# Kernel optimization log

Measured on AMD Instinct MI355X. Metric: run time of the kernel, lower is better.

Reference implementation:

```python
import jax, jax.numpy as jnp
import numpy as np

B, N, H = 2, 4096, 1024
HEADS, DHEAD, M = 16, 64, 256
KERNEL_EPS = 1e-3


def setup_inputs() -> dict:
    key = jax.random.key(0)
    ks = jax.random.split(key, 10)
    w = lambda k, shp: jax.random.normal(k, shp, dtype=jnp.float32) * 0.02
    return {
        "hidden_states": jax.random.normal(ks[0], (B, N, H), dtype=jnp.float32),
        "Wq": w(ks[1], (H, H)), "bq": jnp.zeros((H,), jnp.float32),
        "Wk": w(ks[2], (H, H)), "bk": jnp.zeros((H,), jnp.float32),
        "Wv": w(ks[3], (H, H)), "bv": jnp.zeros((H,), jnp.float32),
        "Wo": w(ks[4], (H, H)), "bo": jnp.zeros((H,), jnp.float32),
        "proj": jax.random.normal(ks[5], (M, DHEAD), dtype=jnp.float32),
    }


def _split_heads(x):
    b, n, _ = x.shape
    return x.reshape(b, n, HEADS, DHEAD).transpose(0, 2, 1, 3)  # [b,h,n,d]


def _softmax_kernel(data, proj, is_query):
    # data: [b,h,n,d]; proj: [m,d]
    data_normalizer = DHEAD ** (-0.25)
    data_dash = jnp.einsum('bhnd,md->bhnm', data_normalizer * data, proj)
    diag_data = -0.5 * jnp.sum(data * data, axis=-1, keepdims=True)  # [b,h,n,1]
    if is_query:
        # argmax over a size-1 last dim -> stabilizer == diag_data itself
        stab = diag_data
    else:
        stab = jnp.max(diag_data)
    kernel_out = jnp.exp(diag_data + (data_dash - stab))  # exp kernel: exp(h + x)
    return (M ** (-0.5)) * (kernel_out + KERNEL_EPS)


def _performer_forward(hidden_states, Wq, bq, Wk, bk, Wv, bv, Wo, bo, proj):
    q = _split_heads(jnp.einsum('bni,oi->bno', hidden_states, Wq) + bq)
    k = _split_heads(jnp.einsum('bni,oi->bno', hidden_states, Wk) + bk)
    v = _split_heads(jnp.einsum('bni,oi->bno', hidden_states, Wv) + bv)

    qf = _softmax_kernel(q, proj, is_query=True)   # [b,h,n,m]
    kf = _softmax_kernel(k, proj, is_query=False)  # [b,h,n,m]

    # linear_attention (non-causal FAVOR+)
    k_cumsum = kf.sum(axis=-2)                                   # [b,h,m]
    d_inv = 1.0 / jnp.einsum('bhnm,bhm->bhn', qf, k_cumsum)      # [b,h,n]
    context = jnp.einsum('bhnm,bhne->bhme', kf, v)               # [b,h,m,d]
    out = jnp.einsum('bhme,bhnm,bhn->bhne', context, qf, d_inv)  # [b,h,n,d]

    out = out.transpose(0, 2, 1, 3).reshape(hidden_states.shape[0], -1, H)
    return jnp.einsum('bni,oi->bno', out, Wo) + bo


def reference(hidden_states, Wq, bq, Wk, bk, Wv, bv, Wo, bo, proj):
    return _performer_forward(hidden_states, Wq, bq, Wk, bk, Wv, bv, Wo, bo, proj)
```

## Files before the change

kernel.cpp:

```cpp
#include <hip/hip_runtime.h>
#include <math.h>

#define B_      2
#define N_      4096
#define H_      1024
#define HEADS_  16
#define DH_     64
#define M_      256
#define NSPLIT  8
#define EPAD    80

constexpr float NORMALIZER = 0.35355339059327373f;
constexpr float RATIO      = 0.0625f;
constexpr float KEPS       = 1e-3f;

typedef __bf16 bf16x8 __attribute__((ext_vector_type(8)));
typedef __bf16 bf16x4 __attribute__((ext_vector_type(4)));
typedef float  f32x4  __attribute__((ext_vector_type(4)));

__global__ __launch_bounds__(256) void split_bf16(
    const float* __restrict__ src, __bf16* __restrict__ hi, __bf16* __restrict__ lo)
{
    int i = blockIdx.x * 256 + threadIdx.x;
    float4 v = ((const float4*)src)[i];
    float vv[4] = {v.x, v.y, v.z, v.w};
    bf16x4 h, l;
#pragma unroll
    for (int j = 0; j < 4; ++j) {
        __bf16 hh = (__bf16)vv[j];
        h[j] = hh;
        l[j] = (__bf16)(vv[j] - (float)hh);
    }
    ((bf16x4*)hi)[i] = h;
    ((bf16x4*)lo)[i] = l;
}

__global__ __launch_bounds__(256) void split_w(
    const float* __restrict__ W0, const float* __restrict__ W1,
    const float* __restrict__ W2, const float* __restrict__ W3,
    __bf16* __restrict__ hi, __bf16* __restrict__ lo)
{
    const float* src = W0;
    if (blockIdx.y == 1) src = W1;
    else if (blockIdx.y == 2) src = W2;
    else if (blockIdx.y == 3) src = W3;
    int i = blockIdx.x * 256 + threadIdx.x;
    size_t o = (size_t)blockIdx.y * 262144 + i;
    float4 v = ((const float4*)src)[i];
    float vv[4] = {v.x, v.y, v.z, v.w};
    bf16x4 h, l;
#pragma unroll
    for (int j = 0; j < 4; ++j) {
        __bf16 hh = (__bf16)vv[j];
        h[j] = hh;
        l[j] = (__bf16)(vv[j] - (float)hh);
    }
    ((bf16x4*)hi)[o] = h;
    ((bf16x4*)lo)[o] = l;
}

template<bool BF16OUT>
__global__ __launch_bounds__(512, 4) void gemm_mfma3(
    const __bf16* __restrict__ Ah, const __bf16* __restrict__ Al,
    const __bf16* __restrict__ Bh0, const __bf16* __restrict__ Bl0,
    const __bf16* __restrict__ Bh1, const __bf16* __restrict__ Bl1,
    const __bf16* __restrict__ Bh2, const __bf16* __restrict__ Bl2,
    const float* __restrict__ bi0, const float* __restrict__ bi1, const float* __restrict__ bi2,
    float* __restrict__ C0,
    __bf16* __restrict__ Ch0, __bf16* __restrict__ Cl0,
    __bf16* __restrict__ Ch1, __bf16* __restrict__ Cl1,
    __bf16* __restrict__ Ch2, __bf16* __restrict__ Cl2)
{
    const __bf16* Bh = Bh0; const __bf16* Bl = Bl0; const float* bias = bi0;
    __bf16* Ch = Ch0; __bf16* Cl = Cl0;
    if (blockIdx.z == 1) { Bh = Bh1; Bl = Bl1; bias = bi1; Ch = Ch1; Cl = Cl1; }
    else if (blockIdx.z == 2) { Bh = Bh2; Bl = Bl2; bias = bi2; Ch = Ch2; Cl = Cl2; }

    __shared__ alignas(16) __bf16 lds[2][4][128 * 32];

    const int t    = threadIdx.x;
    const int lane = t & 63;
    const int lm   = lane & 15;
    const int lq   = lane >> 4;
    const int w    = t >> 6;
    const int wm   = (w >> 2) * 64;
    const int wn   = (w & 3) * 32;

    const int wg = blockIdx.x + 8 * blockIdx.y;
    const int sw = (wg & 7) * 64 + (wg >> 3);
    const int n0 = (sw & 7) * 128;
    const int m0 = (sw >> 3) * 128;
    const int K    = 1024;
    const int NK   = 32;

    const int tw = w >> 1;
    const int hw = w & 1;
    const __bf16* mysrc = (tw == 0) ? Ah : (tw == 1) ? Al : (tw == 2) ? Bh : Bl;
    const int     rbase = ((tw < 2) ? m0 : n0) + hw * 64;
    const int rsub   = lane >> 2;
    const int slot   = lane & 3;
    const int schunk = slot ^ ((lane >> 3) & 3);
    const __bf16* gbase = mysrc + (size_t)(rbase + rsub) * K + schunk * 8;

    f32x4 acc[4][2];
#pragma unroll
    for (int i = 0; i < 4; ++i)
#pragma unroll
        for (int j = 0; j < 2; ++j) acc[i][j] = (f32x4){0.f, 0.f, 0.f, 0.f};

    const int swz = (lq ^ ((lm >> 1) & 3)) * 8;

    auto stage = [&](int buf, int k0) {
#pragma unroll
        for (int c = 0; c < 4; ++c) {
            const __bf16* g = gbase + (size_t)c * 16 * K + k0;
            __builtin_amdgcn_global_load_lds(
                (const __attribute__((address_space(1))) void*)g,
                (__attribute__((address_space(3))) void*)&lds[buf][tw][(hw * 64 + c * 16) * 32],
                16, 0, 0);
        }
    };

    auto compute = [&](int p) {
        const __bf16* tAh = lds[p][0];
        const __bf16* tAl = lds[p][1];
        const __bf16* tBh = lds[p][2];
        const __bf16* tBl = lds[p][3];
        bf16x8 bh[2], bl[2];
#pragma unroll
        for (int j = 0; j < 2; ++j) {
            int off = (wn + j * 16 + lm) * 32 + swz;
            bh[j] = *(const bf16x8*)&tBh[off];
            bl[j] = *(const bf16x8*)&tBl[off];
        }
#pragma unroll
        for (int i = 0; i < 4; ++i) {
            int off = (wm + i * 16 + lm) * 32 + swz;
            bf16x8 ah = *(const bf16x8*)&tAh[off];
            bf16x8 al = *(const bf16x8*)&tAl[off];
#pragma unroll
            for (int j = 0; j < 2; ++j) {
                acc[i][j] = __builtin_amdgcn_mfma_f32_16x16x32_bf16(ah, bh[j], acc[i][j], 0, 0, 0);
                acc[i][j] = __builtin_amdgcn_mfma_f32_16x16x32_bf16(al, bh[j], acc[i][j], 0, 0, 0);
                acc[i][j] = __builtin_amdgcn_mfma_f32_16x16x32_bf16(ah, bl[j], acc[i][j], 0, 0, 0);
            }
        }
    };

    stage(0, 0);
    int p = 0;
#pragma unroll 1
    for (int kk = 0; kk < NK - 1; ++kk) {
        stage(p ^ 1, (kk + 1) * 32);
        asm volatile("s_waitcnt vmcnt(4)" ::: "memory");
        asm volatile("s_barrier" ::: "memory");
        compute(p);
        asm volatile("s_barrier" ::: "memory");
        p ^= 1;
    }
    asm volatile("s_waitcnt vmcnt(0)" ::: "memory");
    asm volatile("s_barrier" ::: "memory");
    compute(p);

    float bsr[2];
#pragma unroll
    for (int j = 0; j < 2; ++j) bsr[j] = bias[n0 + wn + j * 16 + lm];
#pragma unroll
    for (int i = 0; i < 4; ++i)
#pragma unroll
        for (int r = 0; r < 4; ++r) {
            int rowm = m0 + wm + i * 16 + lq * 4 + r;
#pragma unroll
            for (int j = 0; j < 2; ++j) {
                int col = n0 + wn + j * 16 + lm;
                float o = acc[i][j][r] + bsr[j];
                if (BF16OUT) {
                    __bf16 hh = (__bf16)o;
                    Ch[(size_t)rowm * 1024 + col] = hh;
                    Cl[(size_t)rowm * 1024 + col] = (__bf16)(o - (float)hh);
                } else {
                    C0[(size_t)rowm * 1024 + col] = o;
                }
            }
        }
}

__global__ __launch_bounds__(256) void diag_kernel(
    const __bf16* __restrict__ Kh, const __bf16* __restrict__ Kl,
    float* __restrict__ diag, float* __restrict__ partials)
{
    int gt = blockIdx.x * 256 + threadIdx.x;
    int r  = gt >> 2;
    int q  = gt & 3;
    const bf16x8* ph = (const bf16x8*)(Kh + (size_t)r * 64 + q * 16);
    const bf16x8* pl = (const bf16x8*)(Kl + (size_t)r * 64 + q * 16);
    float s = 0.f;
#pragma unroll
    for (int i = 0; i < 2; ++i) {
        bf16x8 vh = ph[i], vl = pl[i];
#pragma unroll
        for (int j = 0; j < 8; ++j) {
            float x = (float)vh[j] + (float)vl[j];
            s += x * x;
        }
    }
    s += __shfl_xor(s, 1);
    s += __shfl_xor(s, 2);
    float d = -0.5f * s;
    if (q == 0) {
        int h = r & 15, bn = r >> 4;
        int n = bn & 4095, b = bn >> 12;
        diag[(((size_t)b * 16 + h) << 12) + n] = d;
    }
    __shared__ float red[256];
    red[threadIdx.x] = d;
    __syncthreads();
    for (int s2 = 128; s2 > 0; s2 >>= 1) {
        if (threadIdx.x < s2) red[threadIdx.x] = fmaxf(red[threadIdx.x], red[threadIdx.x + s2]);
        __syncthreads();
    }
    if (threadIdx.x == 0) partials[blockIdx.x] = red[0];
}

__global__ __launch_bounds__(256) void reduce_stab(
    const float* __restrict__ partials, float* __restrict__ stab, int n)
{
    float m = -3.0e38f;
    for (int i = threadIdx.x; i < n; i += 256) m = fmaxf(m, partials[i]);
    __shared__ float red[256];
    red[threadIdx.x] = m;
    __syncthreads();
    for (int s2 = 128; s2 > 0; s2 >>= 1) {
        if (threadIdx.x < s2) red[threadIdx.x] = fmaxf(red[threadIdx.x], red[threadIdx.x + s2]);
        __syncthreads();
    }
    if (threadIdx.x == 0) stab[0] = red[0];
}

__global__ __launch_bounds__(256) void ctx_mfma(
    const __bf16* __restrict__ Kh, const __bf16* __restrict__ Kl,
    const __bf16* __restrict__ Vh, const __bf16* __restrict__ Vl,
    const __bf16* __restrict__ projH, const __bf16* __restrict__ projL,
    const float* __restrict__ diag, const float* __restrict__ stabp,
    float* __restrict__ ctxp)
{
    __shared__ alignas(16) char ldsbuf[59904];
    __shared__ float dg[64];
    __bf16* kfTh = (__bf16*)ldsbuf;
    __bf16* kfTl = kfTh + 9216;
    __bf16* vTh  = kfTl + 9216;
    __bf16* vTl  = vTh + 5760;
    float*  ctxe = (float*)ldsbuf;

    const int t    = threadIdx.x;
    const int lane = t & 63;
    const int w    = t >> 6;
    const int lm   = lane & 15;
    const int lq   = lane >> 4;
    const int bh   = blockIdx.z;
    const int b    = bh >> 4, h = bh & 15;
    const int mh   = blockIdx.y;
    const int slice = blockIdx.x;
    const int mwave = mh * 128 + w * 32;
    const float stab = stabp[0];
    const size_t rowbase = (size_t)b * N_ * H_ + (size_t)h * DH_;
    const float* diag_bh = diag + (size_t)bh * N_;

    for (int idx = t; idx < 16 * 72; idx += 256) {
        int e = 64 + idx / 72, n = idx % 72;
        vTh[e * 72 + n] = (e == 64 && n < 64) ? (__bf16)1.0f : (__bf16)0.0f;
        vTl[e * 72 + n] = (__bf16)0.0f;
    }

    bf16x8 ph[2][2], pl[2][2];
#pragma unroll
    for (int mf = 0; mf < 2; ++mf)
#pragma unroll
        for (int ks = 0; ks < 2; ++ks) {
            size_t pa = (size_t)(mwave + mf * 16 + lm) * 64 + ks * 32 + lq * 8;
            ph[mf][ks] = *(const bf16x8*)(projH + pa);
            pl[mf][ks] = *(const bf16x8*)(projL + pa);
        }

    f32x4 acc[2][5];
#pragma unroll
    for (int mf = 0; mf < 2; ++mf)
#pragma unroll
        for (int ef = 0; ef < 5; ++ef) acc[mf][ef] = (f32x4){0.f, 0.f, 0.f, 0.f};

    for (int tile = 0; tile < 8; ++tile) {
        const int n0 = slice * (N_ / NSPLIT) + tile * 64;
        __syncthreads();

        {
            int nl = t >> 2, dc = (t & 3) * 16;
            size_t va = rowbase + (size_t)(n0 + nl) * H_ + dc;
            bf16x8 v0 = *(const bf16x8*)(Vh + va);
            bf16x8 v1 = *(const bf16x8*)(Vh + va + 8);
            bf16x8 u0 = *(const bf16x8*)(Vl + va);
            bf16x8 u1 = *(const bf16x8*)(Vl + va + 8);
#pragma unroll
            for (int j = 0; j < 8; ++j) {
                vTh[(dc + j) * 72 + nl]     = v0[j];
                vTh[(dc + 8 + j) * 72 + nl] = v1[j];
                vTl[(dc + j) * 72 + nl]     = u0[j];
                vTl[(dc + 8 + j) * 72 + nl] = u1[j];
            }
        }
        if (t < 64) dg[t] = diag_bh[n0 + t] - stab;

        f32x4 dsh[4][2];
#pragma unroll
        for (int nf = 0; nf < 4; ++nf) {
#pragma unroll
            for (int mf = 0; mf < 2; ++mf) dsh[nf][mf] = (f32x4){0.f, 0.f, 0.f, 0.f};
            bf16x8 ah[2], al[2];
#pragma unroll
            for (int ks = 0; ks < 2; ++ks) {
                size_t ka = rowbase + (size_t)(n0 + nf * 16 + lm) * H_ + ks * 32 + lq * 8;
                ah[ks] = *(const bf16x8*)(Kh + ka);
                al[ks] = *(const bf16x8*)(Kl + ka);
            }
#pragma unroll
            for (int mf = 0; mf < 2; ++mf)
#pragma unroll
                for (int ks = 0; ks < 2; ++ks) {
                    dsh[nf][mf] = __builtin_amdgcn_mfma_f32_16x16x32_bf16(ah[ks], ph[mf][ks], dsh[nf][mf], 0, 0, 0);
                    dsh[nf][mf] = __builtin_amdgcn_mfma_f32_16x16x32_bf16(al[ks], ph[mf][ks], dsh[nf][mf], 0, 0, 0);
                    dsh[nf][mf] = __builtin_amdgcn_mfma_f32_16x16x32_bf16(ah[ks], pl[mf][ks], dsh[nf][mf], 0, 0, 0);
                }
        }

        __syncthreads();

#pragma unroll
        for (int nf = 0; nf < 4; ++nf) {
            float4 dgv = *(const float4*)&dg[nf * 16 + lq * 4];
            float dga[4] = {dgv.x, dgv.y, dgv.z, dgv.w};
#pragma unroll
            for (int mf = 0; mf < 2; ++mf) {
                int mrow = w * 32 + mf * 16 + lm;
                bf16x4 vh_, vl_;
#pragma unroll
                for (int r = 0; r < 4; ++r) {
                    float kf = RATIO * (__expf(dga[r] + NORMALIZER * dsh[nf][mf][r]) + KEPS);
                    __bf16 hh = (__bf16)kf;
                    vh_[r] = hh;
                    vl_[r] = (__bf16)(kf - (float)hh);
                }
                int nbase = nf * 16 + lq * 4;
                *(bf16x4*)&kfTh[mrow * 72 + nbase] = vh_;
                *(bf16x4*)&kfTl[mrow * 72 + nbase] = vl_;
            }
        }

#pragma unroll
        for (int ks = 0; ks < 2; ++ks) {
#pragma unroll
            for (int mf = 0; mf < 2; ++mf) {
                bf16x8 af = *(const bf16x8*)&kfTh[(w * 32 + mf * 16 + lm) * 72 + ks * 32 + lq * 8];
                bf16x8 afl = *(const bf16x8*)&kfTl[(w * 32 + mf * 16 + lm) * 72 + ks * 32 + lq * 8];
#pragma unroll
                for (int ef = 0; ef < 5; ++ef) {
                    bf16x8 bfh = *(const bf16x8*)&vTh[(ef * 16 + lm) * 72 + ks * 32 + lq * 8];
                    bf16x8 bfl = *(const bf16x8*)&vTl[(ef * 16 + lm) * 72 + ks * 32 + lq * 8];
                    acc[mf][ef] = __builtin_amdgcn_mfma_f32_16x16x32_bf16(af,  bfh, acc[mf][ef], 0, 0, 0);
                    acc[mf][ef] = __builtin_amdgcn_mfma_f32_16x16x32_bf16(afl, bfh, acc[mf][ef], 0, 0, 0);
                    acc[mf][ef] = __builtin_amdgcn_mfma_f32_16x16x32_bf16(af,  bfl, acc[mf][ef], 0, 0, 0);
                }
            }
        }
    }

    __syncthreads();
#pragma unroll
    for (int mf = 0; mf < 2; ++mf)
#pragma unroll
        for (int ef = 0; ef < 5; ++ef)
#pragma unroll
            for (int r = 0; r < 4; ++r) {
                int ml = w * 32 + mf * 16 + lq * 4 + r;
                int e  = ef * 16 + lm;
                ctxe[ml * 81 + e] = acc[mf][ef][r];
            }
    __syncthreads();
    const size_t SLICE = (size_t)(B_ * HEADS_) * EPAD * M_;
    const size_t obase = (size_t)slice * SLICE + (size_t)bh * EPAD * M_;
    for (int i = t; i < EPAD * 128; i += 256) {
        int e = i >> 7, ml = i & 127;
        ctxp[obase + (size_t)e * M_ + mh * 128 + ml] = ctxe[ml * 81 + e];
    }
}

__global__ __launch_bounds__(256) void ctx_reduce(
    const float* __restrict__ ctxp, __bf16* __restrict__ ctxTh, __bf16* __restrict__ ctxTl)
{
    int idx = blockIdx.x * 256 + threadIdx.x;
    const size_t SLICE = (size_t)(B_ * HEADS_) * EPAD * M_;
    float s = 0.f;
#pragma unroll
    for (int k = 0; k < NSPLIT; ++k) s += ctxp[(size_t)k * SLICE + idx];
    __bf16 hh = (__bf16)s;
    ctxTh[idx] = hh;
    ctxTl[idx] = (__bf16)(s - (float)hh);
}

__global__ __launch_bounds__(256) void out_mfma(
    const __bf16* __restrict__ Qh, const __bf16* __restrict__ Ql,
    const __bf16* __restrict__ projH, const __bf16* __restrict__ projL,
    const __bf16* __restrict__ ctxTh, const __bf16* __restrict__ ctxTl,
    __bf16* __restrict__ attnH, __bf16* __restrict__ attnL)
{
    __shared__ alignas(16) __bf16 qfh[4][16][72];
    __shared__ alignas(16) __bf16 qfl[4][16][72];

    const int t    = threadIdx.x;
    const int lane = t & 63;
    const int w    = t >> 6;
    const int lm   = lane & 15;
    const int lq   = lane >> 4;
    const int bh   = blockIdx.y;
    const int b    = bh >> 4, h = bh & 15;
    const int nw   = blockIdx.x * 64 + w * 16;
    const size_t rowbase = (size_t)b * N_ * H_ + (size_t)h * DH_;

    bf16x8 qh_[2], ql_[2];
#pragma unroll
    for (int ks = 0; ks < 2; ++ks) {
        size_t qa = rowbase + (size_t)(nw + lm) * H_ + ks * 32 + lq * 8;
        qh_[ks] = *(const bf16x8*)(Qh + qa);
        ql_[ks] = *(const bf16x8*)(Ql + qa);
    }

    const __bf16* cth = ctxTh + (size_t)bh * EPAD * M_;
    const __bf16* ctl = ctxTl + (size_t)bh * EPAD * M_;

    f32x4 accO[5];
#pragma unroll
    for (int ef = 0; ef < 5; ++ef) accO[ef] = (f32x4){0.f, 0.f, 0.f, 0.f};

    for (int mc = 0; mc < 4; ++mc) {
        const int m0 = mc * 64;
        f32x4 dsh[4];
#pragma unroll
        for (int mf = 0; mf < 4; ++mf) {
            dsh[mf] = (f32x4){0.f, 0.f, 0.f, 0.f};
#pragma unroll
            for (int ks = 0; ks < 2; ++ks) {
                size_t pa = (size_t)(m0 + mf * 16 + lm) * 64 + ks * 32 + lq * 8;
                bf16x8 ph = *(const bf16x8*)(projH + pa);
                bf16x8 pl = *(const bf16x8*)(projL + pa);
                dsh[mf] = __builtin_amdgcn_mfma_f32_16x16x32_bf16(qh_[ks], ph, dsh[mf], 0, 0, 0);
                dsh[mf] = __builtin_amdgcn_mfma_f32_16x16x32_bf16(ql_[ks], ph, dsh[mf], 0, 0, 0);
                dsh[mf] = __builtin_amdgcn_mfma_f32_16x16x32_bf16(qh_[ks], pl, dsh[mf], 0, 0, 0);
            }
        }
#pragma unroll
        for (int mf = 0; mf < 4; ++mf)
#pragma unroll
            for (int r = 0; r < 4; ++r) {
                float qf = RATIO * (__expf(NORMALIZER * dsh[mf][r]) + KEPS);
                __bf16 hh = (__bf16)qf;
                int nloc = lq * 4 + r;
                qfh[w][nloc][mf * 16 + lm] = hh;
                qfl[w][nloc][mf * 16 + lm] = (__bf16)(qf - (float)hh);
            }
#pragma unroll
        for (int ks = 0; ks < 2; ++ks) {
            bf16x8 af  = *(const bf16x8*)&qfh[w][lm][ks * 32 + lq * 8];
            bf16x8 afl = *(const bf16x8*)&qfl[w][lm][ks * 32 + lq * 8];
#pragma unroll
            for (int ef = 0; ef < 5; ++ef) {
                size_t ca = (size_t)(ef * 16 + lm) * M_ + m0 + ks * 32 + lq * 8;
                bf16x8 bfh = *(const bf16x8*)(cth + ca);
                bf16x8 bfl = *(const bf16x8*)(ctl + ca);
                accO[ef] = __builtin_amdgcn_mfma_f32_16x16x32_bf16(af,  bfh, accO[ef], 0, 0, 0);
                accO[ef] = __builtin_amdgcn_mfma_f32_16x16x32_bf16(afl, bfh, accO[ef], 0, 0, 0);
                accO[ef] = __builtin_amdgcn_mfma_f32_16x16x32_bf16(af,  bfl, accO[ef], 0, 0, 0);
            }
        }
    }

    float dinv[4];
#pragma unroll
    for (int r = 0; r < 4; ++r) {
        float den = __shfl(accO[4][r], lane & 48);
        dinv[r] = 1.f / den;
    }
#pragma unroll
    for (int ef = 0; ef < 4; ++ef)
#pragma unroll
        for (int r = 0; r < 4; ++r) {
            float o = accO[ef][r] * dinv[r];
            __bf16 hh = (__bf16)o;
            size_t oa = rowbase + (size_t)(nw + lq * 4 + r) * H_ + ef * 16 + lm;
            attnH[oa] = hh;
            attnL[oa] = (__bf16)(o - (float)hh);
        }
}

extern "C" void kernel_launch(void* const* d_in, const int* in_sizes, int n_in,
                              void* d_out, int out_size, void* d_ws, size_t ws_size,
                              hipStream_t stream) {
    const float* hs   = (const float*)d_in[0];
    const float* Wq   = (const float*)d_in[1];
    const float* bq   = (const float*)d_in[2];
    const float* Wk   = (const float*)d_in[3];
    const float* bk   = (const float*)d_in[4];
    const float* Wv   = (const float*)d_in[5];
    const float* bv   = (const float*)d_in[6];
    const float* Wo   = (const float*)d_in[7];
    const float* bo   = (const float*)d_in[8];
    const float* proj = (const float*)d_in[9];
    float* out = (float*)d_out;

    const size_t QSZ = (size_t)B_ * N_ * H_;
    const size_t WSZ = (size_t)H_ * H_;
    const size_t CTXT = (size_t)B_ * HEADS_ * EPAD * M_;

    __bf16* Qh  = (__bf16*)d_ws;
    __bf16* Ql  = Qh + QSZ;
    __bf16* Kh  = Ql + QSZ;
    __bf16* Kl  = Kh + QSZ;
    __bf16* Vh  = Kl + QSZ;
    __bf16* Vl  = Vh + QSZ;
    __bf16* hsH = Vl + QSZ;
    __bf16* hsL = hsH + QSZ;
    __bf16* WH  = hsL + QSZ;
    __bf16* WL  = WH + 4 * WSZ;
    __bf16* projH = WL + 4 * WSZ;
    __bf16* projL = projH + (size_t)M_ * DH_;
    __bf16* ctxTh = projL + (size_t)M_ * DH_;
    __bf16* ctxTl = ctxTh + CTXT;
    float*  diag  = (float*)(ctxTl + CTXT);
    float*  parts = diag + (size_t)B_ * HEADS_ * N_;
    float*  stab  = parts + 2048;
    float*  ctxp  = stab + 16;

    __bf16 *WqH = WH, *WkH = WH + WSZ, *WvH = WH + 2*WSZ, *WoH = WH + 3*WSZ;
    __bf16 *WqL = WL, *WkL = WL + WSZ, *WvL = WL + 2*WSZ, *WoL = WL + 3*WSZ;

    split_bf16<<<QSZ / 4 / 256, 256, 0, stream>>>(hs, hsH, hsL);
    split_w<<<dim3(WSZ / 4 / 256, 4), 256, 0, stream>>>(Wq, Wk, Wv, Wo, WH, WL);
    split_bf16<<<(M_ * DH_) / 4 / 256, 256, 0, stream>>>(proj, projH, projL);

    gemm_mfma3<true><<<dim3(H_ / 128, (B_ * N_) / 128, 3), 512, 0, stream>>>(
        hsH, hsL, WqH, WqL, WkH, WkL, WvH, WvL, bq, bk, bv,
        nullptr, Qh, Ql, Kh, Kl, Vh, Vl);

    diag_kernel<<<2048, 256, 0, stream>>>(Kh, Kl, diag, parts);
    reduce_stab<<<1, 256, 0, stream>>>(parts, stab, 2048);

    ctx_mfma<<<dim3(NSPLIT, 2, B_ * HEADS_), 256, 0, stream>>>(
        Kh, Kl, Vh, Vl, projH, projL, diag, stab, ctxp);

    ctx_reduce<<<(B_ * HEADS_ * EPAD * M_) / 256, 256, 0, stream>>>(ctxp, ctxTh, ctxTl);

    out_mfma<<<dim3(N_ / 64, B_ * HEADS_), 256, 0, stream>>>(
        Qh, Ql, projH, projL, ctxTh, ctxTl, hsH, hsL);

    gemm_mfma3<false><<<dim3(H_ / 128, (B_ * N_) / 128, 1), 512, 0, stream>>>(
        hsH, hsL, WoH, WoL, WoH, WoL, WoH, WoL, bo, bo, bo,
        out, nullptr, nullptr, nullptr, nullptr, nullptr, nullptr);
}
```

Measured before the change: 494.8 us.

## Prefetch next V tile in ctx kernel and double rows per wave in out_mfma

In ctx_mfma, the V tile for the next iteration is loaded into registers after the second barrier, so the global load latency overlaps the exp/kf computation instead of stalling at the start of each tile. In out_mfma, each wave now handles 32 query rows instead of 16, so proj and context fragments loaded from global memory are reused across two row fragments and the grid is halved. This raises register and LDS use per block, which may lower occupancy.

```diff
diff --git a/kernel.cpp b/kernel.cpp
--- a/kernel.cpp
+++ b/kernel.cpp
@@ -288,24 +288,26 @@
 #pragma unroll
         for (int ef = 0; ef < 5; ++ef) acc[mf][ef] = (f32x4){0.f, 0.f, 0.f, 0.f};
 
+    const int nl = t >> 2, dc = (t & 3) * 16;
+    bf16x8 v0, v1, u0, u1;
+    {
+        size_t va = rowbase + (size_t)(slice * (N_ / NSPLIT) + nl) * H_ + dc;
+        v0 = *(const bf16x8*)(Vh + va);
+        v1 = *(const bf16x8*)(Vh + va + 8);
+        u0 = *(const bf16x8*)(Vl + va);
+        u1 = *(const bf16x8*)(Vl + va + 8);
+    }
+
     for (int tile = 0; tile < 8; ++tile) {
         const int n0 = slice * (N_ / NSPLIT) + tile * 64;
         __syncthreads();
 
-        {
-            int nl = t >> 2, dc = (t & 3) * 16;
-            size_t va = rowbase + (size_t)(n0 + nl) * H_ + dc;
-            bf16x8 v0 = *(const bf16x8*)(Vh + va);
-            bf16x8 v1 = *(const bf16x8*)(Vh + va + 8);
-            bf16x8 u0 = *(const bf16x8*)(Vl + va);
-            bf16x8 u1 = *(const bf16x8*)(Vl + va + 8);
-#pragma unroll
-            for (int j = 0; j < 8; ++j) {
-                vTh[(dc + j) * 72 + nl]     = v0[j];
-                vTh[(dc + 8 + j) * 72 + nl] = v1[j];
-                vTl[(dc + j) * 72 + nl]     = u0[j];
-                vTl[(dc + 8 + j) * 72 + nl] = u1[j];
-            }
+#pragma unroll
+        for (int j = 0; j < 8; ++j) {
+            vTh[(dc + j) * 72 + nl]     = v0[j];
+            vTh[(dc + 8 + j) * 72 + nl] = v1[j];
+            vTl[(dc + j) * 72 + nl]     = u0[j];
+            vTl[(dc + 8 + j) * 72 + nl] = u1[j];
         }
         if (t < 64) dg[t] = diag_bh[n0 + t] - stab;
 
@@ -332,6 +334,14 @@
         }
 
         __syncthreads();
+
+        if (tile < 7) {
+            size_t va = rowbase + (size_t)(n0 + 64 + nl) * H_ + dc;
+            v0 = *(const bf16x8*)(Vh + va);
+            v1 = *(const bf16x8*)(Vh + va + 8);
+            u0 = *(const bf16x8*)(Vl + va);
+            u1 = *(const bf16x8*)(Vl + va + 8);
+        }
 
 #pragma unroll
         for (int nf = 0; nf < 4; ++nf) {
@@ -411,8 +421,8 @@
     const __bf16* __restrict__ ctxTh, const __bf16* __restrict__ ctxTl,
     __bf16* __restrict__ attnH, __bf16* __restrict__ attnL)
 {
-    __shared__ alignas(16) __bf16 qfh[4][16][72];
-    __shared__ alignas(16) __bf16 qfl[4][16][72];
+    __shared__ alignas(16) __bf16 qfh[4][32][72];
+    __shared__ alignas(16) __bf16 qfl[4][32][72];
 
     const int t    = threadIdx.x;
     const int lane = t & 63;
@@ -421,82 +431,103 @@
     const int lq   = lane >> 4;
     const int bh   = blockIdx.y;
     const int b    = bh >> 4, h = bh & 15;
-    const int nw   = blockIdx.x * 64 + w * 16;
+    const int nw   = blockIdx.x * 128 + w * 32;
     const size_t rowbase = (size_t)b * N_ * H_ + (size_t)h * DH_;
 
-    bf16x8 qh_[2], ql_[2];
-#pragma unroll
-    for (int ks = 0; ks < 2; ++ks) {
-        size_t qa = rowbase + (size_t)(nw + lm) * H_ + ks * 32 + lq * 8;
-        qh_[ks] = *(const bf16x8*)(Qh + qa);
-        ql_[ks] = *(const bf16x8*)(Ql + qa);
-    }
+    bf16x8 qh_[2][2], ql_[2][2];
+#pragma unroll
+    for (int nf = 0; nf < 2; ++nf)
+#pragma unroll
+        for (int ks = 0; ks < 2; ++ks) {
+            size_t qa = rowbase + (size_t)(nw + nf * 16 + lm) * H_ + ks * 32 + lq * 8;
+            qh_[nf][ks] = *(const bf16x8*)(Qh + qa);
+            ql_[nf][ks] = *(const bf16x8*)(Ql + qa);
+        }
 
     const __bf16* cth = ctxTh + (size_t)bh * EPAD * M_;
     const __bf16* ctl = ctxTl + (size_t)bh * EPAD * M_;
 
-    f32x4 accO[5];
-#pragma unroll
-    for (int ef = 0; ef < 5; ++ef) accO[ef] = (f32x4){0.f, 0.f, 0.f, 0.f};
+    f32x4 accO[2][5];
+#pragma unroll
+    for (int nf = 0; nf < 2; ++nf)
+#pragma unroll
+        for (int ef = 0; ef < 5; ++ef) accO[nf][ef] = (f32x4){0.f, 0.f, 0.f, 0.f};
 
     for (int mc = 0; mc < 4; ++mc) {
         const int m0 = mc * 64;
-        f32x4 dsh[4];
-#pragma unroll
-        for (int mf = 0; mf < 4; ++mf) {
-            dsh[mf] = (f32x4){0.f, 0.f, 0.f, 0.f};
+        f32x4 dsh[2][4];
+#pragma unroll
+        for (int nf = 0; nf < 2; ++nf)
+#pragma unroll
+            for (int mf = 0; mf < 4; ++mf) dsh[nf][mf] = (f32x4){0.f, 0.f, 0.f, 0.f};
+#pragma unroll
+        for (int mf = 0; mf < 4; ++mf)
 #pragma unroll
             for (int ks = 0; ks < 2; ++ks) {
                 size_t pa = (size_t)(m0 + mf * 16 + lm) * 64 + ks * 32 + lq * 8;
                 bf16x8 ph = *(const bf16x8*)(projH + pa);
                 bf16x8 pl = *(const bf16x8*)(projL + pa);
-                dsh[mf] = __builtin_amdgcn_mfma_f32_16x16x32_bf16(qh_[ks], ph, dsh[mf], 0, 0, 0);
-                dsh[mf] = __builtin_amdgcn_mfma_f32_16x16x32_bf16(ql_[ks], ph, dsh[mf], 0, 0, 0);
-                dsh[mf] = __builtin_amdgcn_mfma_f32_16x16x32_bf16(qh_[ks], pl, dsh[mf], 0, 0, 0);
-            }
-        }
-#pragma unroll
-        for (int mf = 0; mf < 4; ++mf)
-#pragma unroll
-            for (int r = 0; r < 4; ++r) {
-                float qf = RATIO * (__expf(NORMALIZER * dsh[mf][r]) + KEPS);
-                __bf16 hh = (__bf16)qf;
-                int nloc = lq * 4 + r;
-                qfh[w][nloc][mf * 16 + lm] = hh;
-                qfl[w][nloc][mf * 16 + lm] = (__bf16)(qf - (float)hh);
-            }
+#pragma unroll
+                for (int nf = 0; nf < 2; ++nf) {
+                    dsh[nf][mf] = __builtin_amdgcn_mfma_f32_16x16x32_bf16(qh_[nf][ks], ph, dsh[nf][mf], 0, 0, 0);
+                    dsh[nf][mf] = __builtin_amdgcn_mfma_f32_16x16x32_bf16(ql_[nf][ks], ph, dsh[nf][mf], 0, 0, 0);
+                    dsh[nf][mf] = __builtin_amdgcn_mfma_f32_16x16x32_bf16(qh_[nf][ks], pl, dsh[nf][mf], 0, 0, 0);
+                }
+            }
+#pragma unroll
+        for (int nf = 0; nf < 2; ++nf)
+#pragma unroll
+            for (int mf = 0; mf < 4; ++mf)
+#pragma unroll
+                for (int r = 0; r < 4; ++r) {
+                    float qf = RATIO * (__expf(NORMALIZER * dsh[nf][mf][r]) + KEPS);
+                    __bf16 hh = (__bf16)qf;
+                    int nloc = nf * 16 + lq * 4 + r;
+                    qfh[w][nloc][mf * 16 + lm] = hh;
+                    qfl[w][nloc][mf * 16 + lm] = (__bf16)(qf - (float)hh);
+                }
 #pragma unroll
         for (int ks = 0; ks < 2; ++ks) {
-            bf16x8 af  = *(const bf16x8*)&qfh[w][lm][ks * 32 + lq * 8];
-            bf16x8 afl = *(const bf16x8*)&qfl[w][lm][ks * 32 + lq * 8];
+            bf16x8 af[2], afl[2];
+#pragma unroll
+            for (int nf = 0; nf < 2; ++nf) {
+                af[nf]  = *(const bf16x8*)&qfh[w][nf * 16 + lm][ks * 32 + lq * 8];
+                afl[nf] = *(const bf16x8*)&qfl[w][nf * 16 + lm][ks * 32 + lq * 8];
+            }
 #pragma unroll
             for (int ef = 0; ef < 5; ++ef) {
                 size_t ca = (size_t)(ef * 16 + lm) * M_ + m0 + ks * 32 + lq * 8;
                 bf16x8 bfh = *(const bf16x8*)(cth + ca);
                 bf16x8 bfl = *(const bf16x8*)(ctl + ca);
-                accO[ef] = __builtin_amdgcn_mfma_f32_16x16x32_bf16(af,  bfh, accO[ef], 0, 0, 0);
-                accO[ef] = __builtin_amdgcn_mfma_f32_16x16x32_bf16(afl, bfh, accO[ef], 0, 0, 0);
-                accO[ef] = __builtin_amdgcn_mfma_f32_16x16x32_bf16(af,  bfl, accO[ef], 0, 0, 0);
-            }
-        }
-    }
-
-    float dinv[4];
-#pragma unroll
-    for (int r = 0; r < 4; ++r) {
-        float den = __shfl(accO[4][r], lane & 48);
-        dinv[r] = 1.f / den;
-    }
-#pragma unroll
-    for (int ef = 0; ef < 4; ++ef)
+#pragma unroll
+                for (int nf = 0; nf < 2; ++nf) {
+                    accO[nf][ef] = __builtin_amdgcn_mfma_f32_16x16x32_bf16(af[nf],  bfh, accO[nf][ef], 0, 0, 0);
+                    accO[nf][ef] = __builtin_amdgcn_mfma_f32_16x16x32_bf16(afl[nf], bfh, accO[nf][ef], 0, 0, 0);
+                    accO[nf][ef] = __builtin_amdgcn_mfma_f32_16x16x32_bf16(af[nf],  bfl, accO[nf][ef], 0, 0, 0);
+                }
+            }
+        }
+    }
+
+#pragma unroll
+    for (int nf = 0; nf < 2; ++nf) {
+        float dinv[4];
 #pragma unroll
         for (int r = 0; r < 4; ++r) {
-            float o = accO[ef][r] * dinv[r];
-            __bf16 hh = (__bf16)o;
-            size_t oa = rowbase + (size_t)(nw + lq * 4 + r) * H_ + ef * 16 + lm;
-            attnH[oa] = hh;
-            attnL[oa] = (__bf16)(o - (float)hh);
-        }
+            float den = __shfl(accO[nf][4][r], lane & 48);
+            dinv[r] = 1.f / den;
+        }
+#pragma unroll
+        for (int ef = 0; ef < 4; ++ef)
+#pragma unroll
+            for (int r = 0; r < 4; ++r) {
+                float o = accO[nf][ef][r] * dinv[r];
+                __bf16 hh = (__bf16)o;
+                size_t oa = rowbase + (size_t)(nw + nf * 16 + lq * 4 + r) * H_ + ef * 16 + lm;
+                attnH[oa] = hh;
+                attnL[oa] = (__bf16)(o - (float)hh);
+            }
+    }
 }
 
 extern "C" void kernel_launch(void* const* d_in, const int* in_sizes, int n_in,
@@ -556,7 +587,7 @@
 
     ctx_reduce<<<(B_ * HEADS_ * EPAD * M_) / 256, 256, 0, stream>>>(ctxp, ctxTh, ctxTl);
 
-    out_mfma<<<dim3(N_ / 64, B_ * HEADS_), 256, 0, stream>>>(
+    out_mfma<<<dim3(N_ / 128, B_ * HEADS_), 256, 0, stream>>>(
         Qh, Ql, projH, projL, ctxTh, ctxTl, hsH, hsL);
 
     gemm_mfma3<false><<<dim3(H_ / 128, (B_ * N_) / 128, 1), 512, 0, stream>>>(
```

Measured after the change: 451.5 us. 1.1x faster.
